# Kernel tuning notes

Measured on AMD Instinct MI355X. Metric: run time of the kernel, lower is better.

## Reference

```python
import jax, jax.numpy as jnp
import numpy as np

N_NODES = 50000
N_EDGES = 800000
IN_DIM = 128
HID_DIM = 128
OUT_DIM = 128


def gcn_conv(x, src, dst, W, b, n):
    """PyG-style GCNConv: linear, add self-loops, sym-normalized scatter-add."""
    h = x @ W  # [N, out]
    loop = jnp.arange(n, dtype=src.dtype)
    src_f = jnp.concatenate([src, loop])
    dst_f = jnp.concatenate([dst, loop])
    ones = jnp.ones(src_f.shape[0], dtype=h.dtype)
    deg = jax.ops.segment_sum(ones, dst_f, num_segments=n)  # in-degree incl. self-loop
    dinv = jnp.where(deg > 0, jax.lax.rsqrt(deg), 0.0)
    norm = dinv[src_f] * dinv[dst_f]  # [E+N]
    msg = h[src_f] * norm[:, None]  # gather + scale
    out = jax.ops.segment_sum(msg, dst_f, num_segments=n)  # scatter-add
    return out + b


def setup_inputs() -> dict:
    key = jax.random.key(0)
    k1, k2, k3, k4, k5, k6 = jax.random.split(key, 6)
    posts = jax.random.normal(k1, (N_NODES, IN_DIM), dtype=jnp.float32)
    edge_index = jax.random.randint(k2, (2, N_EDGES), 0, N_NODES, dtype=jnp.int32)
    root_index = 0
    s1 = 1.0 / np.sqrt(IN_DIM)
    s2 = 1.0 / np.sqrt(HID_DIM + IN_DIM)
    W1 = jax.random.uniform(k3, (IN_DIM, HID_DIM), jnp.float32, -s1, s1)
    b1 = jax.random.uniform(k4, (HID_DIM,), jnp.float32, -s1, s1)
    W2 = jax.random.uniform(k5, (HID_DIM + IN_DIM, OUT_DIM), jnp.float32, -s2, s2)
    b2 = jax.random.uniform(k6, (OUT_DIM,), jnp.float32, -s2, s2)
    return {"posts": posts, "edge_index": edge_index, "root_index": root_index,
            "W1": W1, "b1": b1, "W2": W2, "b2": b2}


def reference(posts, edge_index, root_index, W1, b1, W2, b2):
    n = posts.shape[0]
    src, dst = edge_index[0], edge_index[1]
    post_root = posts[root_index]  # [in_dim], broadcast to all nodes below
    conv1_out = gcn_conv(posts, src, dst, W1, b1, n)  # [N, hid]
    conv1_root = conv1_out[root_index]  # [hid]
    conv2_in = jnp.concatenate(
        [jnp.broadcast_to(post_root, (n, post_root.shape[0])), conv1_out], axis=1)
    conv2_in = jax.nn.relu(conv2_in)  # dropout is identity in eval mode
    conv2_out = jax.nn.relu(gcn_conv(conv2_in, src, dst, W2, b2, n))  # [N, out]
    # mean over nodes of cat([conv1_root broadcast, conv2_out])
    feature = jnp.concatenate([conv1_root, jnp.mean(conv2_out, axis=0)])
    return feature.reshape(1, -1)
```

## Files before the change

kernel.cpp:

```cpp
#include <hip/hip_runtime.h>

#define DIM 128
typedef unsigned int uint;
typedef unsigned short ushort;

#define RFL __builtin_amdgcn_readfirstlane

__device__ __forceinline__ ushort f2bf(float x) {
    uint u = __float_as_uint(x);
    u = u + 0x7FFFu + ((u >> 16) & 1u);
    return (ushort)(u >> 16);
}
__device__ __forceinline__ uint pack2(float a, float b) {
    return (uint)f2bf(a) | ((uint)f2bf(b) << 16);
}

__global__ __launch_bounds__(256) void k_count(const int* __restrict__ dst,
                                               int* __restrict__ deg, int E) {
    int t = blockIdx.x * 256 + threadIdx.x;
    if (t < E) atomicAdd(&deg[dst[t]], 1);
}

__global__ __launch_bounds__(256) void k_dinv(const int* __restrict__ deg,
                                              float* __restrict__ dinv, int N) {
    int t = blockIdx.x * 256 + threadIdx.x;
    if (t < N) dinv[t] = rsqrtf((float)(deg[t] + 1));
}

__global__ __launch_bounds__(256) void k_scanA(const int* __restrict__ deg,
                                               int* __restrict__ rowptr,
                                               int* __restrict__ segsum, int N) {
    int i = blockIdx.x * 256 + threadIdx.x;
    int v = (i < N) ? deg[i] : 0;
    __shared__ int ps[256];
    ps[threadIdx.x] = v;
    __syncthreads();
    for (int off = 1; off < 256; off <<= 1) {
        int u = (threadIdx.x >= off) ? ps[threadIdx.x - off] : 0;
        __syncthreads();
        ps[threadIdx.x] += u;
        __syncthreads();
    }
    if (i < N) rowptr[i] = ps[threadIdx.x] - v;
    if (threadIdx.x == 255) segsum[blockIdx.x] = ps[255];
}

__global__ __launch_bounds__(256) void k_scanB(int* __restrict__ segsum, int nseg) {
    int t = threadIdx.x;
    int v = (t < nseg) ? segsum[t] : 0;
    __shared__ int ps[256];
    ps[t] = v;
    __syncthreads();
    for (int off = 1; off < 256; off <<= 1) {
        int u = (t >= off) ? ps[t - off] : 0;
        __syncthreads();
        ps[t] += u;
        __syncthreads();
    }
    if (t < nseg) segsum[t] = ps[t] - v;
}

__global__ __launch_bounds__(256) void k_scanC(int* __restrict__ rowptr,
                                               const int* __restrict__ segsum,
                                               int* __restrict__ cursor, int N, int E) {
    int i = blockIdx.x * 256 + threadIdx.x;
    if (i < N) {
        int r = rowptr[i] + segsum[blockIdx.x];
        rowptr[i] = r;
        cursor[i] = r;
    }
    if (i == 0) rowptr[N] = E;
}

__global__ __launch_bounds__(256) void k_fill(const int* __restrict__ src,
                                              const int* __restrict__ dst,
                                              const float* __restrict__ dinv,
                                              int* __restrict__ cursor,
                                              int2* __restrict__ csr, int E) {
    int e = blockIdx.x * 256 + threadIdx.x;
    if (e >= E) return;
    int s = src[e], d = dst[e];
    int p = atomicAdd(&cursor[d], 1);
    float w = dinv[s] * dinv[d];
    csr[p] = make_int2(s, __float_as_int(w));
}

template<bool RELU_IN, bool ADD_C>
__global__ __launch_bounds__(256) void k_gemm(const float* __restrict__ X,
                                              const float* __restrict__ W,
                                              const float* __restrict__ Cvec,
                                              ushort* __restrict__ H, int n) {
    __shared__ float sW[64 * DIM];
    __shared__ float sX[32][DIM];
    const int jq = threadIdx.x & 31;
    const int rr = threadIdx.x >> 5;
    float4 cj = ADD_C ? ((const float4*)Cvec)[jq] : make_float4(0.f, 0.f, 0.f, 0.f);
    for (int base = blockIdx.x * 32; base < n; base += gridDim.x * 32) {
        __syncthreads();
        for (int u = threadIdx.x; u < 32 * 32; u += 256) {
            int row = u >> 5, c4 = u & 31;
            int gi = base + row;
            float4 v = make_float4(0.f, 0.f, 0.f, 0.f);
            if (gi < n) v = ((const float4*)(X + (size_t)gi * DIM))[c4];
            if (RELU_IN) {
                v.x = fmaxf(v.x, 0.f); v.y = fmaxf(v.y, 0.f);
                v.z = fmaxf(v.z, 0.f); v.w = fmaxf(v.w, 0.f);
            }
            ((float4*)sX[row])[c4] = v;
        }
        float4 a0 = cj, a1 = cj, a2 = cj, a3 = cj;
        for (int kk = 0; kk < DIM; kk += 64) {
            __syncthreads();
            for (int u = threadIdx.x; u < 64 * 32; u += 256)
                ((float4*)sW)[u] = ((const float4*)(W + (size_t)kk * DIM))[u];
            __syncthreads();
            #pragma unroll 8
            for (int k2 = 0; k2 < 64; ++k2) {
                int k = kk + k2;
                float4 w4 = ((const float4*)sW)[k2 * 32 + jq];
                float x0 = sX[rr * 4 + 0][k], x1 = sX[rr * 4 + 1][k];
                float x2 = sX[rr * 4 + 2][k], x3 = sX[rr * 4 + 3][k];
                a0.x = fmaf(x0, w4.x, a0.x); a0.y = fmaf(x0, w4.y, a0.y);
                a0.z = fmaf(x0, w4.z, a0.z); a0.w = fmaf(x0, w4.w, a0.w);
                a1.x = fmaf(x1, w4.x, a1.x); a1.y = fmaf(x1, w4.y, a1.y);
                a1.z = fmaf(x1, w4.z, a1.z); a1.w = fmaf(x1, w4.w, a1.w);
                a2.x = fmaf(x2, w4.x, a2.x); a2.y = fmaf(x2, w4.y, a2.y);
                a2.z = fmaf(x2, w4.z, a2.z); a2.w = fmaf(x2, w4.w, a2.w);
                a3.x = fmaf(x3, w4.x, a3.x); a3.y = fmaf(x3, w4.y, a3.y);
                a3.z = fmaf(x3, w4.z, a3.z); a3.w = fmaf(x3, w4.w, a3.w);
            }
        }
        int i0 = base + rr * 4;
        if (i0 + 0 < n) ((uint2*)(H + (size_t)(i0 + 0) * DIM))[jq] =
            make_uint2(pack2(a0.x, a0.y), pack2(a0.z, a0.w));
        if (i0 + 1 < n) ((uint2*)(H + (size_t)(i0 + 1) * DIM))[jq] =
            make_uint2(pack2(a1.x, a1.y), pack2(a1.z, a1.w));
        if (i0 + 2 < n) ((uint2*)(H + (size_t)(i0 + 2) * DIM))[jq] =
            make_uint2(pack2(a2.x, a2.y), pack2(a2.z, a2.w));
        if (i0 + 3 < n) ((uint2*)(H + (size_t)(i0 + 3) * DIM))[jq] =
            make_uint2(pack2(a3.x, a3.y), pack2(a3.z, a3.w));
    }
}

__global__ __launch_bounds__(DIM) void k_cvec(const float* __restrict__ posts,
                                              const int* __restrict__ root,
                                              const float* __restrict__ W2,
                                              float* __restrict__ cvec) {
    int j = threadIdx.x;
    const float* xr = posts + (size_t)root[0] * DIM;
    float acc = 0.0f;
    #pragma unroll 8
    for (int k = 0; k < DIM; ++k)
        acc = fmaf(fmaxf(xr[k], 0.0f), W2[k * DIM + j], acc);
    cvec[j] = acc;
}

__device__ __forceinline__ void wave_accum(const int2* __restrict__ csr,
                                           int beg, int end, int q,
                                           const ushort* __restrict__ h,
                                           float& a0, float& a1) {
    int e = beg;
    for (; e + 16 <= end; e += 16) {
        int sc[16];
        float wt[16];
        #pragma unroll
        for (int u = 0; u < 16; ++u) {
            int2 c = csr[e + u];
            sc[u] = RFL(c.x);
            wt[u] = __int_as_float(RFL(c.y));
        }
        uint hv[16];
        #pragma unroll
        for (int u = 0; u < 16; ++u)
            hv[u] = ((const uint*)(h + (size_t)sc[u] * DIM))[q];
        #pragma unroll
        for (int u = 0; u < 16; ++u) {
            a0 = fmaf(__uint_as_float(hv[u] << 16), wt[u], a0);
            a1 = fmaf(__uint_as_float(hv[u] & 0xFFFF0000u), wt[u], a1);
        }
    }
    for (; e + 8 <= end; e += 8) {
        int sc[8];
        float wt[8];
        #pragma unroll
        for (int u = 0; u < 8; ++u) {
            int2 c = csr[e + u];
            sc[u] = RFL(c.x);
            wt[u] = __int_as_float(RFL(c.y));
        }
        uint hv[8];
        #pragma unroll
        for (int u = 0; u < 8; ++u)
            hv[u] = ((const uint*)(h + (size_t)sc[u] * DIM))[q];
        #pragma unroll
        for (int u = 0; u < 8; ++u) {
            a0 = fmaf(__uint_as_float(hv[u] << 16), wt[u], a0);
            a1 = fmaf(__uint_as_float(hv[u] & 0xFFFF0000u), wt[u], a1);
        }
    }
    int rem = end - e;
    if (rem > 0) {
        int sc[8];
        float wt[8];
        #pragma unroll
        for (int u = 0; u < 8; ++u) {
            int idx = e + u; idx = idx < end ? idx : end - 1;
            int2 c = csr[idx];
            sc[u] = RFL(c.x);
            wt[u] = (u < rem) ? __int_as_float(RFL(c.y)) : 0.f;
        }
        uint hv[8];
        #pragma unroll
        for (int u = 0; u < 8; ++u)
            hv[u] = ((const uint*)(h + (size_t)sc[u] * DIM))[q];
        #pragma unroll
        for (int u = 0; u < 8; ++u) {
            a0 = fmaf(__uint_as_float(hv[u] << 16), wt[u], a0);
            a1 = fmaf(__uint_as_float(hv[u] & 0xFFFF0000u), wt[u], a1);
        }
    }
}

__global__ __launch_bounds__(256) void k_gather1(const int2* __restrict__ csr,
                                                 const int* __restrict__ rowptr,
                                                 const float* __restrict__ dinv,
                                                 const ushort* __restrict__ h,
                                                 const float* __restrict__ b1,
                                                 const int* __restrict__ root,
                                                 float* __restrict__ conv1,
                                                 float* __restrict__ out, int N) {
    int q = threadIdx.x & 63;
    int wid = blockIdx.x * 4 + (threadIdx.x >> 6);
    int wstride = gridDim.x * 4;
    float2 bv = ((const float2*)b1)[q];
    int rt = RFL(root[0]);
    for (int d = wid; d < N; d += wstride) {
        int beg = RFL(rowptr[d]);
        int end = RFL(rowptr[d + 1]);
        float a0 = 0.f, a1 = 0.f;
        wave_accum(csr, beg, end, q, h, a0, a1);
        float di = dinv[d], sl = di * di;
        uint hv = ((const uint*)(h + (size_t)d * DIM))[q];
        float2 r;
        r.x = fmaf(__uint_as_float(hv << 16), sl, a0) + bv.x;
        r.y = fmaf(__uint_as_float(hv & 0xFFFF0000u), sl, a1) + bv.y;
        ((float2*)(conv1 + (size_t)d * DIM))[q] = r;
        if (d == rt) ((float2*)out)[q] = r;
    }
}

__global__ __launch_bounds__(256) void k_gather2(const int2* __restrict__ csr,
                                                 const int* __restrict__ rowptr,
                                                 const float* __restrict__ dinv,
                                                 const ushort* __restrict__ h,
                                                 const float* __restrict__ b2,
                                                 float* __restrict__ meanacc, int N) {
    int q = threadIdx.x & 63;
    int wid = blockIdx.x * 4 + (threadIdx.x >> 6);
    int wstride = gridDim.x * 4;
    float2 bv = ((const float2*)b2)[q];
    float s0 = 0.f, s1 = 0.f;
    for (int d = wid; d < N; d += wstride) {
        int beg = RFL(rowptr[d]);
        int end = RFL(rowptr[d + 1]);
        float a0 = 0.f, a1 = 0.f;
        wave_accum(csr, beg, end, q, h, a0, a1);
        float di = dinv[d], sl = di * di;
        uint hv = ((const uint*)(h + (size_t)d * DIM))[q];
        s0 += fmaxf(fmaf(__uint_as_float(hv << 16), sl, a0) + bv.x, 0.f);
        s1 += fmaxf(fmaf(__uint_as_float(hv & 0xFFFF0000u), sl, a1) + bv.y, 0.f);
    }
    __shared__ float2 sp[256];
    sp[threadIdx.x] = make_float2(s0, s1);
    __syncthreads();
    if (threadIdx.x < 64) {
        float2 s = sp[threadIdx.x];
        #pragma unroll
        for (int g = 1; g < 4; ++g) {
            float2 o = sp[g * 64 + threadIdx.x];
            s.x += o.x; s.y += o.y;
        }
        unsafeAtomicAdd(&meanacc[q * 2 + 0], s.x);
        unsafeAtomicAdd(&meanacc[q * 2 + 1], s.y);
    }
}

__global__ __launch_bounds__(DIM) void k_reduce(const float* __restrict__ meanacc,
                                                float* __restrict__ out, int N) {
    int j = threadIdx.x;
    out[DIM + j] = meanacc[j] / (float)N;
}

extern "C" void kernel_launch(void* const* d_in, const int* in_sizes, int n_in,
                              void* d_out, int out_size, void* d_ws, size_t ws_size,
                              hipStream_t stream) {
    const float* posts = (const float*)d_in[0];
    const int*   eidx  = (const int*)d_in[1];
    const int*   root  = (const int*)d_in[2];
    const float* W1    = (const float*)d_in[3];
    const float* b1    = (const float*)d_in[4];
    const float* W2    = (const float*)d_in[5];
    const float* b2    = (const float*)d_in[6];
    float* out = (float*)d_out;

    int N = in_sizes[0] / DIM;
    int E = in_sizes[1] / 2;
    const int* src = eidx;
    const int* dst = eidx + E;
    int nseg = (N + 255) / 256;

    char* ws = (char*)d_ws;
    size_t off = 0;
    auto alloc = [&](size_t bytes) {
        void* p = ws + off;
        off += (bytes + 511) & ~(size_t)511;
        return p;
    };
    int*    deg     = (int*)   alloc((size_t)N * 4);
    int*    rowptr  = (int*)   alloc((size_t)(N + 1) * 4);
    int*    cursor  = (int*)   alloc((size_t)N * 4);
    int*    segsum  = (int*)   alloc((size_t)nseg * 4);
    float*  dinv    = (float*) alloc((size_t)N * 4);
    float*  cvec    = (float*) alloc(DIM * 4);
    float*  meanacc = (float*) alloc(DIM * 4);
    int2*   csr     = (int2*)  alloc((size_t)E * 8);
    ushort* h       = (ushort*)alloc((size_t)N * DIM * 2);
    float*  conv1   = (float*) alloc((size_t)N * DIM * 4);

    hipMemsetAsync(deg, 0, (size_t)N * 4, stream);
    hipMemsetAsync(meanacc, 0, DIM * 4, stream);

    k_count<<<(E + 255) / 256, 256, 0, stream>>>(dst, deg, E);
    k_scanA<<<nseg, 256, 0, stream>>>(deg, rowptr, segsum, N);
    k_scanB<<<1, 256, 0, stream>>>(segsum, nseg);
    k_scanC<<<nseg, 256, 0, stream>>>(rowptr, segsum, cursor, N, E);
    k_dinv<<<(N + 255) / 256, 256, 0, stream>>>(deg, dinv, N);
    k_fill<<<(E + 255) / 256, 256, 0, stream>>>(src, dst, dinv, cursor, csr, E);

    k_gemm<false, false><<<512, 256, 0, stream>>>(posts, W1, nullptr, h, N);
    k_gather1<<<2048, 256, 0, stream>>>(csr, rowptr, dinv, h, b1, root, conv1, out, N);

    k_cvec<<<1, DIM, 0, stream>>>(posts, root, W2, cvec);
    k_gemm<true, true><<<512, 256, 0, stream>>>(conv1, W2 + DIM * DIM, cvec, h, N);
    k_gather2<<<2048, 256, 0, stream>>>(csr, rowptr, dinv, h, b2, meanacc, N);
    k_reduce<<<1, DIM, 0, stream>>>(meanacc, out, N);
}
```

Baseline: 332.5 us.

## Use bf16 MFMA with LDS-resident transposed weights in the node GEMM

Replaces the scalar FP32 FMA GEMM with a bf16 MFMA 16x16x32 kernel. The block converts the full 128x128 weight matrix to bf16 once, transposed into padded shared memory, and each wave computes a 16-row tile of outputs. The grid is halved to 256 blocks. This aims to cut the GEMM compute cost, at the price of rounding inputs and weights to bf16, scattered 2-byte output stores, and extra per-block weight setup.

```diff
diff --git a/kernel.cpp b/kernel.cpp
--- a/kernel.cpp
+++ b/kernel.cpp
@@ -1,18 +1,19 @@
 #include <hip/hip_runtime.h>
 
 #define DIM 128
+#define WPAD 136
 typedef unsigned int uint;
 typedef unsigned short ushort;
 
 #define RFL __builtin_amdgcn_readfirstlane
+
+typedef __attribute__((ext_vector_type(8))) short bf16x8;
+typedef __attribute__((ext_vector_type(4))) float f32x4;
 
 __device__ __forceinline__ ushort f2bf(float x) {
     uint u = __float_as_uint(x);
     u = u + 0x7FFFu + ((u >> 16) & 1u);
     return (ushort)(u >> 16);
-}
-__device__ __forceinline__ uint pack2(float a, float b) {
-    return (uint)f2bf(a) | ((uint)f2bf(b) << 16);
 }
 
 __global__ __launch_bounds__(256) void k_count(const int* __restrict__ dst,
@@ -90,55 +91,60 @@
                                               const float* __restrict__ W,
                                               const float* __restrict__ Cvec,
                                               ushort* __restrict__ H, int n) {
-    __shared__ float sW[64 * DIM];
-    __shared__ float sX[32][DIM];
-    const int jq = threadIdx.x & 31;
-    const int rr = threadIdx.x >> 5;
-    float4 cj = ADD_C ? ((const float4*)Cvec)[jq] : make_float4(0.f, 0.f, 0.f, 0.f);
-    for (int base = blockIdx.x * 32; base < n; base += gridDim.x * 32) {
-        __syncthreads();
-        for (int u = threadIdx.x; u < 32 * 32; u += 256) {
-            int row = u >> 5, c4 = u & 31;
-            int gi = base + row;
+    __shared__ ushort sWT[DIM][WPAD];
+    __shared__ ushort sX[4][16][WPAD];
+    const int tid = threadIdx.x;
+    const int w = tid >> 6, l = tid & 63;
+    const int col = l & 15;
+    const int kg = l >> 4;
+
+    for (int idx = tid; idx < DIM * DIM; idx += 256) {
+        int k = idx >> 7, j = idx & 127;
+        sWT[j][k] = f2bf(W[idx]);
+    }
+    float cj[8];
+    if (ADD_C) {
+        #pragma unroll
+        for (int t = 0; t < 8; ++t) cj[t] = Cvec[t * 16 + col];
+    }
+    __syncthreads();
+
+    for (int base = blockIdx.x * 64; base < n; base += gridDim.x * 64) {
+        int i0 = base + w * 16;
+        for (int idx = l; idx < 16 * 32; idx += 64) {
+            int r = idx >> 5, c4 = idx & 31;
             float4 v = make_float4(0.f, 0.f, 0.f, 0.f);
-            if (gi < n) v = ((const float4*)(X + (size_t)gi * DIM))[c4];
+            if (i0 + r < n) v = ((const float4*)(X + (size_t)(i0 + r) * DIM))[c4];
             if (RELU_IN) {
                 v.x = fmaxf(v.x, 0.f); v.y = fmaxf(v.y, 0.f);
                 v.z = fmaxf(v.z, 0.f); v.w = fmaxf(v.w, 0.f);
             }
-            ((float4*)sX[row])[c4] = v;
-        }
-        float4 a0 = cj, a1 = cj, a2 = cj, a3 = cj;
-        for (int kk = 0; kk < DIM; kk += 64) {
-            __syncthreads();
-            for (int u = threadIdx.x; u < 64 * 32; u += 256)
-                ((float4*)sW)[u] = ((const float4*)(W + (size_t)kk * DIM))[u];
-            __syncthreads();
-            #pragma unroll 8
-            for (int k2 = 0; k2 < 64; ++k2) {
-                int k = kk + k2;
-                float4 w4 = ((const float4*)sW)[k2 * 32 + jq];
-                float x0 = sX[rr * 4 + 0][k], x1 = sX[rr * 4 + 1][k];
-                float x2 = sX[rr * 4 + 2][k], x3 = sX[rr * 4 + 3][k];
-                a0.x = fmaf(x0, w4.x, a0.x); a0.y = fmaf(x0, w4.y, a0.y);
-                a0.z = fmaf(x0, w4.z, a0.z); a0.w = fmaf(x0, w4.w, a0.w);
-                a1.x = fmaf(x1, w4.x, a1.x); a1.y = fmaf(x1, w4.y, a1.y);
-                a1.z = fmaf(x1, w4.z, a1.z); a1.w = fmaf(x1, w4.w, a1.w);
-                a2.x = fmaf(x2, w4.x, a2.x); a2.y = fmaf(x2, w4.y, a2.y);
-                a2.z = fmaf(x2, w4.z, a2.z); a2.w = fmaf(x2, w4.w, a2.w);
-                a3.x = fmaf(x3, w4.x, a3.x); a3.y = fmaf(x3, w4.y, a3.y);
-                a3.z = fmaf(x3, w4.z, a3.z); a3.w = fmaf(x3, w4.w, a3.w);
+            ushort* p = &sX[w][r][c4 * 4];
+            p[0] = f2bf(v.x); p[1] = f2bf(v.y); p[2] = f2bf(v.z); p[3] = f2bf(v.w);
+        }
+        f32x4 acc[8];
+        #pragma unroll
+        for (int t = 0; t < 8; ++t) {
+            float c0 = ADD_C ? cj[t] : 0.f;
+            acc[t][0] = c0; acc[t][1] = c0; acc[t][2] = c0; acc[t][3] = c0;
+        }
+        #pragma unroll
+        for (int k0 = 0; k0 < DIM; k0 += 32) {
+            bf16x8 a = *(const bf16x8*)&sX[w][col][k0 + kg * 8];
+            #pragma unroll
+            for (int t = 0; t < 8; ++t) {
+                bf16x8 b = *(const bf16x8*)&sWT[t * 16 + col][k0 + kg * 8];
+                acc[t] = __builtin_amdgcn_mfma_f32_16x16x32_bf16(a, b, acc[t], 0, 0, 0);
             }
         }
-        int i0 = base + rr * 4;
-        if (i0 + 0 < n) ((uint2*)(H + (size_t)(i0 + 0) * DIM))[jq] =
-            make_uint2(pack2(a0.x, a0.y), pack2(a0.z, a0.w));
-        if (i0 + 1 < n) ((uint2*)(H + (size_t)(i0 + 1) * DIM))[jq] =
-            make_uint2(pack2(a1.x, a1.y), pack2(a1.z, a1.w));
-        if (i0 + 2 < n) ((uint2*)(H + (size_t)(i0 + 2) * DIM))[jq] =
-            make_uint2(pack2(a2.x, a2.y), pack2(a2.z, a2.w));
-        if (i0 + 3 < n) ((uint2*)(H + (size_t)(i0 + 3) * DIM))[jq] =
-            make_uint2(pack2(a3.x, a3.y), pack2(a3.z, a3.w));
+        #pragma unroll
+        for (int t = 0; t < 8; ++t) {
+            #pragma unroll
+            for (int r = 0; r < 4; ++r) {
+                int row = i0 + kg * 4 + r;
+                if (row < n) H[(size_t)row * DIM + t * 16 + col] = f2bf(acc[t][r]);
+            }
+        }
     }
 }
 
@@ -337,11 +343,11 @@
     k_dinv<<<(N + 255) / 256, 256, 0, stream>>>(deg, dinv, N);
     k_fill<<<(E + 255) / 256, 256, 0, stream>>>(src, dst, dinv, cursor, csr, E);
 
-    k_gemm<false, false><<<512, 256, 0, stream>>>(posts, W1, nullptr, h, N);
+    k_gemm<false, false><<<256, 256, 0, stream>>>(posts, W1, nullptr, h, N);
     k_gather1<<<2048, 256, 0, stream>>>(csr, rowptr, dinv, h, b1, root, conv1, out, N);
 
     k_cvec<<<1, DIM, 0, stream>>>(posts, root, W2, cvec);
-    k_gemm<true, true><<<512, 256, 0, stream>>>(conv1, W2 + DIM * DIM, cvec, h, N);
+    k_gemm<true, true><<<256, 256, 0, stream>>>(conv1, W2 + DIM * DIM, cvec, h, N);
     k_gather2<<<2048, 256, 0, stream>>>(csr, rowptr, dinv, h, b2, meanacc, N);
     k_reduce<<<1, DIM, 0, stream>>>(meanacc, out, N);
 }
```

New measurement: 302.9 us (median of 2 runs). 8.9% less time.
